# Kernel optimization log

Measured on AMD Instinct MI355X. Metric: run time of the kernel, lower is better.

Reference implementation:

```python
import jax, jax.numpy as jnp
import numpy as np

ALPHA = 0.5  # config_param['alpha']


def setup_inputs() -> dict:
    key = jax.random.key(0)
    ks = jax.random.split(key, 10)
    B, T, N, E, H = 64, 20, 8192, 128, 128
    # sparse multi-hot basket indicators
    x = (jax.random.uniform(ks[0], (B, T, N)) < 0.01).astype(jnp.float32)
    seq_len = jax.random.randint(ks[1], (B,), 1, T + 1)  # pack_padded requires >=1
    A = jax.random.uniform(ks[2], (N, N), dtype=jnp.float32) * 0.01  # dense item-item adjacency
    W1 = jax.random.normal(ks[3], (E, N), dtype=jnp.float32) * 0.02
    b1 = jnp.zeros((E,), jnp.float32)
    W2 = jax.random.normal(ks[4], (E, N), dtype=jnp.float32) * 0.02
    b2 = jnp.zeros((E,), jnp.float32)
    W_ih = jax.random.normal(ks[5], (4 * H, E), dtype=jnp.float32) * 0.05
    W_hh = jax.random.normal(ks[6], (4 * H, H), dtype=jnp.float32) * 0.05
    b_ih = jnp.zeros((4 * H,), jnp.float32)
    b_hh = jnp.zeros((4 * H,), jnp.float32)
    W_out = jax.random.normal(ks[7], (N, H), dtype=jnp.float32) * 0.02
    I_B = jnp.ones((N,), jnp.float32) / N  # item_probs-style bias init
    threshold = jnp.array([0.005], jnp.float32)  # adj_matrix.mean()
    return dict(x=x, seq_len=seq_len, A=A, W1=W1, b1=b1, W2=W2, b2=b2,
                W_ih=W_ih, W_hh=W_hh, b_ih=b_ih, b_hh=b_hh,
                W_out=W_out, I_B=I_B, threshold=threshold)


def reference(x, seq_len, A, W1, b1, W2, b2, W_ih, W_hh, b_ih, b_hh, W_out, I_B, threshold):
    B, T, N = x.shape
    H = W_hh.shape[1]
    xf = x.reshape(B * T, N)
    # two basket encoders, elementwise max combine (dropout = identity in eval)
    e1 = jax.nn.relu(xf @ W1.T + b1)
    e2 = jax.nn.relu(xf @ W2.T + b2)
    basket = jnp.maximum(e1, e2).reshape(B, T, -1)  # [B, T, E]

    # 1-layer LSTM (torch gate order i,f,g,o); packed variable-length seqs
    # emulated by freezing (h, c) once t >= seq_len, so h_n matches pack_padded.
    valid = jnp.arange(T)[:, None] < seq_len[None, :]  # [T, B]
    xs = basket.transpose(1, 0, 2)                     # [T, B, E]
    b = b_ih + b_hh

    def step(carry, inp):
        h, c = carry
        x_t, v = inp
        gates = x_t @ W_ih.T + h @ W_hh.T + b
        i, f, g, o = jnp.split(gates, 4, axis=-1)
        c_new = jax.nn.sigmoid(f) * c + jax.nn.sigmoid(i) * jnp.tanh(g)
        h_new = jax.nn.sigmoid(o) * jnp.tanh(c_new)
        m = v[:, None]
        return (jnp.where(m, h_new, h), jnp.where(m, c_new, c)), None

    h0 = jnp.zeros((B, H), x.dtype)
    c0 = jnp.zeros((B, H), x.dtype)
    (h_n, _), _ = jax.lax.scan(step, (h0, c0), (xs, valid))

    p = jax.nn.sigmoid(h_n @ W_out.T)  # [B, N]
    # mm(p, diag(relu(I_B))) is algebraically an elementwise scale
    predict = (1.0 - ALPHA) * p + ALPHA * (p * jax.nn.relu(I_B) + jax.nn.relu(p @ A))
    return predict
```

## Files before the change

kernel.cpp:

```cpp
#include <hip/hip_runtime.h>
#include <hip/hip_bf16.h>
#include <stdint.h>

#define B_ 64
#define T_ 20
#define N_ 8192
#define E_ 128
#define H_ 128
#define G4 512
#define SPLITK 8

typedef short bf16x8 __attribute__((ext_vector_type(8)));
typedef float f32x4 __attribute__((ext_vector_type(4)));

__device__ __forceinline__ float sigmoidf_(float x){ return 1.0f/(1.0f+expf(-x)); }

__device__ __forceinline__ unsigned short f2bf(float f){
  union { float f; uint32_t u; } v; v.f = f;
  uint32_t u = v.u;
  uint32_t r = (u + 0x7FFFu + ((u >> 16) & 1u)) >> 16;
  return (unsigned short)r;
}
__device__ __forceinline__ uint32_t pk2(float a, float b){
  return (uint32_t)f2bf(a) | ((uint32_t)f2bf(b) << 16);
}
__device__ __forceinline__ float bf2f(unsigned short s){
  union { uint32_t u; float f; } v; v.u = ((uint32_t)s) << 16; return v.f;
}

__global__ void k_transpose(const float* __restrict__ W1, const float* __restrict__ W2,
                            unsigned short* __restrict__ W12T){
  __shared__ float t1[128][33];
  __shared__ float t2[128][33];
  int n0 = blockIdx.x * 32;
  int tid = threadIdx.x;
  int nl = tid & 31, eg = tid >> 5;
  for (int i = 0; i < 16; i++){
    int e = eg * 16 + i;
    t1[e][nl] = W1[(size_t)e*N_ + n0 + nl];
    t2[e][nl] = W2[(size_t)e*N_ + n0 + nl];
  }
  __syncthreads();
  for (int n = 0; n < 32; n++){
    float v = (tid < 128) ? t1[tid][n] : t2[tid-128][n];
    W12T[(size_t)(n0+n)*256 + tid] = f2bf(v);
  }
}

__global__ void k_mlp(const float* __restrict__ x, const int* __restrict__ seq_len,
                      const unsigned short* __restrict__ W12T, const float* __restrict__ b1,
                      const float* __restrict__ b2, float* __restrict__ basket){
  int bt = blockIdx.x;
  int b = bt / T_, t = bt % T_;
  int tid = threadIdx.x;
  if (t >= seq_len[b]){
    if (tid < 128) basket[(size_t)bt*E_ + tid] = 0.f;
    return;
  }
  __shared__ int idxs[1024];
  __shared__ int cnt;
  __shared__ float e2s[128];
  if (tid == 0) cnt = 0;
  __syncthreads();
  const float4* xr = (const float4*)(x + (size_t)bt * N_);
  for (int i = 0; i < 8; i++){
    float4 v = xr[i*256 + tid];
    int base = (i*256 + tid)*4;
    if (v.x != 0.f){ int q = atomicAdd(&cnt,1); idxs[q] = base;   }
    if (v.y != 0.f){ int q = atomicAdd(&cnt,1); idxs[q] = base+1; }
    if (v.z != 0.f){ int q = atomicAdd(&cnt,1); idxs[q] = base+2; }
    if (v.w != 0.f){ int q = atomicAdd(&cnt,1); idxs[q] = base+3; }
  }
  __syncthreads();
  int m = cnt; if (m > 1024) m = 1024;
  float acc = (tid < 128) ? b1[tid] : b2[tid-128];
  int i = 0;
  for (; i + 8 <= m; i += 8){
    int j0 = idxs[i+0], j1 = idxs[i+1], j2 = idxs[i+2], j3 = idxs[i+3];
    int j4 = idxs[i+4], j5 = idxs[i+5], j6 = idxs[i+6], j7 = idxs[i+7];
    float v0 = bf2f(W12T[(size_t)j0*256 + tid]);
    float v1 = bf2f(W12T[(size_t)j1*256 + tid]);
    float v2 = bf2f(W12T[(size_t)j2*256 + tid]);
    float v3 = bf2f(W12T[(size_t)j3*256 + tid]);
    float v4 = bf2f(W12T[(size_t)j4*256 + tid]);
    float v5 = bf2f(W12T[(size_t)j5*256 + tid]);
    float v6 = bf2f(W12T[(size_t)j6*256 + tid]);
    float v7 = bf2f(W12T[(size_t)j7*256 + tid]);
    acc += ((v0+v1)+(v2+v3)) + ((v4+v5)+(v6+v7));
  }
  for (; i < m; i++)
    acc += bf2f(W12T[(size_t)idxs[i]*256 + tid]);
  acc = fmaxf(acc, 0.f);
  if (tid >= 128) e2s[tid-128] = acc;
  __syncthreads();
  if (tid < 128) basket[(size_t)bt*E_ + tid] = fmaxf(acc, e2s[tid]);
}

__global__ void k_xgemm(const float* __restrict__ basket, const float* __restrict__ W_ih,
                        const float* __restrict__ b_ih, const float* __restrict__ b_hh,
                        float* __restrict__ Xp){
  __shared__ unsigned short hb[64*128];
  int tid = threadIdx.x;
  int rt = blockIdx.x;
  int ct = blockIdx.y;
  {
    int row = tid >> 2;
    int k16 = (tid & 3) * 32;
    const float4* hr = (const float4*)(basket + ((size_t)rt*64 + row)*E_ + k16);
    #pragma unroll
    for (int i = 0; i < 4; i++){
      float4 a = hr[i*2], bq = hr[i*2+1];
      uint4 u; u.x = pk2(a.x,a.y); u.y = pk2(a.z,a.w); u.z = pk2(bq.x,bq.y); u.w = pk2(bq.z,bq.w);
      int blk = (k16 >> 3) + i;
      *(uint4*)&hb[row*128 + ((blk ^ (row & 7)) * 8)] = u;
    }
  }
  __syncthreads();
  int w = tid >> 6, l = tid & 63;
  int n0 = ct * 128;
  f32x4 acc[8];
  #pragma unroll
  for (int i = 0; i < 8; i++) acc[i] = (f32x4){0.f,0.f,0.f,0.f};
  int row = w*16 + (l & 15);
  #pragma unroll
  for (int ks = 0; ks < 4; ks++){
    int kk = ks*32 + (l >> 4)*8;
    int blk = kk >> 3;
    bf16x8 af = *(bf16x8*)&hb[row*128 + ((blk ^ (row & 7)) * 8)];
    #pragma unroll
    for (int nt = 0; nt < 8; nt++){
      int n = n0 + nt*16 + (l & 15);
      const float4* wp = (const float4*)(W_ih + (size_t)n*E_ + kk);
      float4 wa = wp[0], wb = wp[1];
      union { uint4 u; bf16x8 v; } cc;
      cc.u.x = pk2(wa.x,wa.y); cc.u.y = pk2(wa.z,wa.w);
      cc.u.z = pk2(wb.x,wb.y); cc.u.w = pk2(wb.z,wb.w);
      acc[nt] = __builtin_amdgcn_mfma_f32_16x16x32_bf16(af, cc.v, acc[nt], 0, 0, 0);
    }
  }
  #pragma unroll
  for (int nt = 0; nt < 8; nt++){
    int n = n0 + nt*16 + (l & 15);
    float bias = b_ih[n] + b_hh[n];
    #pragma unroll
    for (int r = 0; r < 4; r++){
      int rr = w*16 + (l >> 4)*4 + r;
      Xp[((size_t)rt*64 + rr)*G4 + n] = acc[nt][r] + bias;
    }
  }
}

__global__ void __launch_bounds__(512, 2)
k_lstm(const int* __restrict__ seq_len, const float* __restrict__ Xp,
       const float* __restrict__ W_hh, float* __restrict__ hn){
  int b = blockIdx.x;
  int L = seq_len[b];
  int j = threadIdx.x;
  float4 whh[32];
  const float4* wr = (const float4*)(W_hh + (size_t)j * H_);
  #pragma unroll
  for (int k = 0; k < 32; k++) whh[k] = wr[k];
  __shared__ float hs[128];
  __shared__ float gs[512];
  if (j < 128) hs[j] = 0.f;
  float c = 0.f;
  __syncthreads();
  for (int t = 0; t < L; t++){
    float s0 = Xp[((size_t)b*T_ + t)*G4 + j], s1 = 0.f, s2 = 0.f, s3 = 0.f;
    #pragma unroll
    for (int k = 0; k < 32; k += 4){
      float4 w, h;
      w = whh[k+0]; h = *(const float4*)&hs[k*4+ 0]; s0 += w.x*h.x + w.y*h.y + w.z*h.z + w.w*h.w;
      w = whh[k+1]; h = *(const float4*)&hs[k*4+ 4]; s1 += w.x*h.x + w.y*h.y + w.z*h.z + w.w*h.w;
      w = whh[k+2]; h = *(const float4*)&hs[k*4+ 8]; s2 += w.x*h.x + w.y*h.y + w.z*h.z + w.w*h.w;
      w = whh[k+3]; h = *(const float4*)&hs[k*4+12]; s3 += w.x*h.x + w.y*h.y + w.z*h.z + w.w*h.w;
    }
    gs[j] = (s0 + s1) + (s2 + s3);
    __syncthreads();
    if (j < 128){
      float i_ = gs[j], f_ = gs[128+j], gg = gs[256+j], o_ = gs[384+j];
      c = sigmoidf_(f_)*c + sigmoidf_(i_)*tanhf(gg);
      hs[j] = sigmoidf_(o_)*tanhf(c);
    }
    __syncthreads();
  }
  if (j < 128) hn[(size_t)b*H_ + j] = hs[j];
}

__global__ void k_pout(const float* __restrict__ hn, const float* __restrict__ W_out,
                       unsigned short* __restrict__ pbf){
  __shared__ unsigned short hb[64*128];
  int tid = threadIdx.x;
  {
    int row = tid >> 2;
    int k16 = (tid & 3) * 32;
    const float4* hr = (const float4*)(hn + (size_t)row*H_ + k16);
    #pragma unroll
    for (int i = 0; i < 4; i++){
      float4 a = hr[i*2], bq = hr[i*2+1];
      uint4 u; u.x = pk2(a.x,a.y); u.y = pk2(a.z,a.w); u.z = pk2(bq.x,bq.y); u.w = pk2(bq.z,bq.w);
      int blk = (k16 >> 3) + i;
      *(uint4*)&hb[row*128 + ((blk ^ (row & 7)) * 8)] = u;
    }
  }
  __syncthreads();
  int w = tid >> 6, l = tid & 63;
  int n0 = blockIdx.x * 128;
  f32x4 acc[8];
  #pragma unroll
  for (int i = 0; i < 8; i++) acc[i] = (f32x4){0.f,0.f,0.f,0.f};
  int row = w*16 + (l & 15);
  #pragma unroll
  for (int ks = 0; ks < 4; ks++){
    int kk = ks*32 + (l >> 4)*8;
    int blk = kk >> 3;
    bf16x8 af = *(bf16x8*)&hb[row*128 + ((blk ^ (row & 7)) * 8)];
    #pragma unroll
    for (int nt = 0; nt < 8; nt++){
      int n = n0 + nt*16 + (l & 15);
      const float4* wp = (const float4*)(W_out + (size_t)n*H_ + kk);
      float4 wa = wp[0], wb = wp[1];
      union { uint4 u; bf16x8 v; } cc;
      cc.u.x = pk2(wa.x,wa.y); cc.u.y = pk2(wa.z,wa.w);
      cc.u.z = pk2(wb.x,wb.y); cc.u.w = pk2(wb.z,wb.w);
      acc[nt] = __builtin_amdgcn_mfma_f32_16x16x32_bf16(af, cc.v, acc[nt], 0, 0, 0);
    }
  }
  #pragma unroll
  for (int nt = 0; nt < 8; nt++){
    int n = n0 + nt*16 + (l & 15);
    #pragma unroll
    for (int r = 0; r < 4; r++){
      int rr = w*16 + (l >> 4)*4 + r;
      float pv = 1.f/(1.f + expf(-acc[nt][r]));
      pbf[(size_t)rr*N_ + n] = f2bf(pv);
    }
  }
}

__global__ void __launch_bounds__(512, 4)
k_gemm(const unsigned short* __restrict__ pbf, const float* __restrict__ Ag,
       float* __restrict__ Cp){
  __shared__ unsigned short Abf0[128*64];
  __shared__ unsigned short Abf1[128*64];
  __shared__ unsigned short pt0[64*64];
  __shared__ unsigned short pt1[64*64];
  int tid = threadIdx.x;
  int nb = blockIdx.x & 63, ks = blockIdx.x >> 6;
  int n0 = nb * 128;
  int kbase = ks * (N_ / SPLITK);
  int sn = tid & 127, kq = tid >> 7;
  int prow = tid >> 3, c8 = tid & 7;
  int w = tid >> 6, l = tid & 63;
  int wm = w >> 2, wn = w & 3;
  f32x4 acc[2][2];
  #pragma unroll
  for (int i = 0; i < 2; i++)
    #pragma unroll
    for (int q = 0; q < 2; q++) acc[i][q] = (f32x4){0.f,0.f,0.f,0.f};
  float* Cout = Cp + (size_t)ks * (B_ * N_);
  const int NSTEP = (N_ / SPLITK) / 64;

  float aA[16], aB[16];
  uint4 pA, pB;

  auto issue = [&](float* ar, uint4& pr, int kb){
    pr = *(const uint4*)&pbf[(size_t)prow*N_ + kb + c8*8];
    #pragma unroll
    for (int i = 0; i < 4; i++){
      const float* base = Ag + (size_t)(kb + kq*16 + i*4)*N_ + n0 + sn;
      ar[i*4+0] = base[0];
      ar[i*4+1] = base[(size_t)N_];
      ar[i*4+2] = base[(size_t)2*N_];
      ar[i*4+3] = base[(size_t)3*N_];
    }
  };
  auto stage = [&](unsigned short* abf, unsigned short* ptb, const float* ar, const uint4& pr){
    *(uint4*)&ptb[prow*64 + ((c8*8) ^ ((prow & 7)*8))] = pr;
    #pragma unroll
    for (int i = 0; i < 4; i++){
      int k = kq*16 + i*4;
      uint2 u; u.x = pk2(ar[i*4+0], ar[i*4+1]); u.y = pk2(ar[i*4+2], ar[i*4+3]);
      *(uint2*)&abf[sn*64 + (k ^ ((sn & 7)*8))] = u;
    }
  };
  auto compute = [&](const unsigned short* abf, const unsigned short* ptb){
    #pragma unroll
    for (int kc = 0; kc < 64; kc += 32){
      int ko = kc + (l >> 4)*8;
      bf16x8 af[2], bfr[2];
      #pragma unroll
      for (int mi = 0; mi < 2; mi++){
        int r = wm*32 + mi*16 + (l & 15);
        af[mi] = *(const bf16x8*)&ptb[r*64 + (ko ^ ((r & 7)*8))];
      }
      #pragma unroll
      for (int ni = 0; ni < 2; ni++){
        int n = wn*32 + ni*16 + (l & 15);
        bfr[ni] = *(const bf16x8*)&abf[n*64 + (ko ^ ((n & 7)*8))];
      }
      #pragma unroll
      for (int mi = 0; mi < 2; mi++)
        #pragma unroll
        for (int ni = 0; ni < 2; ni++)
          acc[mi][ni] = __builtin_amdgcn_mfma_f32_16x16x32_bf16(af[mi], bfr[ni], acc[mi][ni], 0, 0, 0);
    }
  };

  issue(aA, pA, kbase);
  for (int s = 0; s < NSTEP; s += 2){
    if (s + 1 < NSTEP) issue(aB, pB, kbase + (s+1)*64);
    stage(Abf0, pt0, aA, pA);
    asm volatile("s_waitcnt lgkmcnt(0)" ::: "memory");
    __builtin_amdgcn_sched_barrier(0);
    __builtin_amdgcn_s_barrier();
    __builtin_amdgcn_sched_barrier(0);
    compute(Abf0, pt0);
    if (s + 2 < NSTEP) issue(aA, pA, kbase + (s+2)*64);
    stage(Abf1, pt1, aB, pB);
    asm volatile("s_waitcnt lgkmcnt(0)" ::: "memory");
    __builtin_amdgcn_sched_barrier(0);
    __builtin_amdgcn_s_barrier();
    __builtin_amdgcn_sched_barrier(0);
    compute(Abf1, pt1);
  }

  #pragma unroll
  for (int mi = 0; mi < 2; mi++)
    #pragma unroll
    for (int ni = 0; ni < 2; ni++){
      int n = n0 + wn*32 + ni*16 + (l & 15);
      #pragma unroll
      for (int r = 0; r < 4; r++){
        int rr = wm*32 + mi*16 + (l >> 4)*4 + r;
        Cout[(size_t)rr*N_ + n] = acc[mi][ni][r];
      }
    }
}

__global__ void k_final(const unsigned short* __restrict__ pbf, const float* __restrict__ Cp,
                        const float* __restrict__ I_B, float* __restrict__ out){
  int idx = blockIdx.x*256 + threadIdx.x;
  ushort4 pu = ((const ushort4*)pbf)[idx];
  float4 cv = {0.f, 0.f, 0.f, 0.f};
  #pragma unroll
  for (int s = 0; s < SPLITK; s++){
    float4 v = ((const float4*)(Cp + (size_t)s * (B_ * N_)))[idx];
    cv.x += v.x; cv.y += v.y; cv.z += v.z; cv.w += v.w;
  }
  int n = (idx*4) & (N_-1);
  float4 ib = *(const float4*)&I_B[n];
  float4 o;
  float p0 = bf2f(pu.x), p1 = bf2f(pu.y), p2 = bf2f(pu.z), p3 = bf2f(pu.w);
  o.x = 0.5f*p0 + 0.5f*(p0*fmaxf(ib.x,0.f) + fmaxf(cv.x,0.f));
  o.y = 0.5f*p1 + 0.5f*(p1*fmaxf(ib.y,0.f) + fmaxf(cv.y,0.f));
  o.z = 0.5f*p2 + 0.5f*(p2*fmaxf(ib.z,0.f) + fmaxf(cv.z,0.f));
  o.w = 0.5f*p3 + 0.5f*(p3*fmaxf(ib.w,0.f) + fmaxf(cv.w,0.f));
  ((float4*)out)[idx] = o;
}

extern "C" void kernel_launch(void* const* d_in, const int* in_sizes, int n_in,
                              void* d_out, int out_size, void* d_ws, size_t ws_size,
                              hipStream_t stream) {
  const float* x     = (const float*)d_in[0];
  const int*   seq   = (const int*)  d_in[1];
  const float* A     = (const float*)d_in[2];
  const float* W1    = (const float*)d_in[3];
  const float* b1    = (const float*)d_in[4];
  const float* W2    = (const float*)d_in[5];
  const float* b2    = (const float*)d_in[6];
  const float* W_ih  = (const float*)d_in[7];
  const float* W_hh  = (const float*)d_in[8];
  const float* b_ih  = (const float*)d_in[9];
  const float* b_hh  = (const float*)d_in[10];
  const float* W_out = (const float*)d_in[11];
  const float* I_B   = (const float*)d_in[12];
  float* out = (float*)d_out;

  float* ws   = (float*)d_ws;
  unsigned short* W12T = (unsigned short*)ws;
  float* basket = ws + 1048576;
  float* Xp     = basket + 163840;
  float* hn     = Xp + 655360;
  float* Cp     = hn + 8192;
  unsigned short* pbf = (unsigned short*)(Cp + 4194304);

  k_transpose<<<256, 256, 0, stream>>>(W1, W2, W12T);
  k_mlp      <<<1280,256, 0, stream>>>(x, seq, W12T, b1, b2, basket);
  k_xgemm    <<<dim3(20,4), 256, 0, stream>>>(basket, W_ih, b_ih, b_hh, Xp);
  k_lstm     <<<64,  512, 0, stream>>>(seq, Xp, W_hh, hn);
  k_pout     <<<64,  256, 0, stream>>>(hn, W_out, pbf);
  k_gemm     <<<64*SPLITK, 512, 0, stream>>>(pbf, A, Cp);
  k_final    <<<512, 256, 0, stream>>>(pbf, Cp, I_B, out);
}
```

Before: 152.5 us.

## Fuse input projection into LSTM kernel and split-K reduction into GEMM

The separate MFMA input-projection GEMM is removed. Each LSTM block now computes its own 20x512 input gates in fp32 from shared-memory basket rows and keeps them in LDS. The final epilogue kernel is folded into the main GEMM through a per-column-tile atomic semaphore, so the last split-K block reduces the partial sums and writes the output. This saves two kernel launches and the Xp round trip through global memory, in exchange for more serial scalar work per LSTM block, heavy register pressure, and a tail reduction done by a few blocks.

```diff
diff --git a/kernel.cpp b/kernel.cpp
--- a/kernel.cpp
+++ b/kernel.cpp
@@ -29,7 +29,8 @@
 }
 
 __global__ void k_transpose(const float* __restrict__ W1, const float* __restrict__ W2,
-                            unsigned short* __restrict__ W12T){
+                            unsigned short* __restrict__ W12T, unsigned* __restrict__ sems){
+  if (blockIdx.x == 0 && threadIdx.x < 64) sems[threadIdx.x] = 0;
   __shared__ float t1[128][33];
   __shared__ float t2[128][33];
   int n0 = blockIdx.x * 32;
@@ -96,77 +97,47 @@
   if (tid < 128) basket[(size_t)bt*E_ + tid] = fmaxf(acc, e2s[tid]);
 }
 
-__global__ void k_xgemm(const float* __restrict__ basket, const float* __restrict__ W_ih,
-                        const float* __restrict__ b_ih, const float* __restrict__ b_hh,
-                        float* __restrict__ Xp){
-  __shared__ unsigned short hb[64*128];
-  int tid = threadIdx.x;
-  int rt = blockIdx.x;
-  int ct = blockIdx.y;
-  {
-    int row = tid >> 2;
-    int k16 = (tid & 3) * 32;
-    const float4* hr = (const float4*)(basket + ((size_t)rt*64 + row)*E_ + k16);
-    #pragma unroll
-    for (int i = 0; i < 4; i++){
-      float4 a = hr[i*2], bq = hr[i*2+1];
-      uint4 u; u.x = pk2(a.x,a.y); u.y = pk2(a.z,a.w); u.z = pk2(bq.x,bq.y); u.w = pk2(bq.z,bq.w);
-      int blk = (k16 >> 3) + i;
-      *(uint4*)&hb[row*128 + ((blk ^ (row & 7)) * 8)] = u;
-    }
-  }
-  __syncthreads();
-  int w = tid >> 6, l = tid & 63;
-  int n0 = ct * 128;
-  f32x4 acc[8];
-  #pragma unroll
-  for (int i = 0; i < 8; i++) acc[i] = (f32x4){0.f,0.f,0.f,0.f};
-  int row = w*16 + (l & 15);
-  #pragma unroll
-  for (int ks = 0; ks < 4; ks++){
-    int kk = ks*32 + (l >> 4)*8;
-    int blk = kk >> 3;
-    bf16x8 af = *(bf16x8*)&hb[row*128 + ((blk ^ (row & 7)) * 8)];
-    #pragma unroll
-    for (int nt = 0; nt < 8; nt++){
-      int n = n0 + nt*16 + (l & 15);
-      const float4* wp = (const float4*)(W_ih + (size_t)n*E_ + kk);
-      float4 wa = wp[0], wb = wp[1];
-      union { uint4 u; bf16x8 v; } cc;
-      cc.u.x = pk2(wa.x,wa.y); cc.u.y = pk2(wa.z,wa.w);
-      cc.u.z = pk2(wb.x,wb.y); cc.u.w = pk2(wb.z,wb.w);
-      acc[nt] = __builtin_amdgcn_mfma_f32_16x16x32_bf16(af, cc.v, acc[nt], 0, 0, 0);
-    }
-  }
-  #pragma unroll
-  for (int nt = 0; nt < 8; nt++){
-    int n = n0 + nt*16 + (l & 15);
-    float bias = b_ih[n] + b_hh[n];
-    #pragma unroll
-    for (int r = 0; r < 4; r++){
-      int rr = w*16 + (l >> 4)*4 + r;
-      Xp[((size_t)rt*64 + rr)*G4 + n] = acc[nt][r] + bias;
-    }
-  }
-}
-
-__global__ void __launch_bounds__(512, 2)
-k_lstm(const int* __restrict__ seq_len, const float* __restrict__ Xp,
-       const float* __restrict__ W_hh, float* __restrict__ hn){
+__global__ void __launch_bounds__(512, 1)
+k_lstmx(const int* __restrict__ seq_len, const float* __restrict__ basket,
+        const float* __restrict__ W_ih, const float* __restrict__ b_ih,
+        const float* __restrict__ b_hh, const float* __restrict__ W_hh,
+        float* __restrict__ hn){
   int b = blockIdx.x;
   int L = seq_len[b];
   int j = threadIdx.x;
-  float4 whh[32];
-  const float4* wr = (const float4*)(W_hh + (size_t)j * H_);
-  #pragma unroll
-  for (int k = 0; k < 32; k++) whh[k] = wr[k];
+  __shared__ float bsk[T_][E_];
+  __shared__ float XpL[T_][G4];
   __shared__ float hs[128];
   __shared__ float gs[512];
+  for (int idx = j; idx < T_*E_; idx += 512)
+    bsk[idx>>7][idx&127] = basket[((size_t)b*T_ + (idx>>7))*E_ + (idx&127)];
+  __syncthreads();
+  {
+    float bias = b_ih[j] + b_hh[j];
+    float accv[T_];
+    #pragma unroll
+    for (int tt = 0; tt < T_; tt++) accv[tt] = bias;
+    const float4* wr = (const float4*)(W_ih + (size_t)j * E_);
+    for (int k4 = 0; k4 < 32; k4++){
+      float4 w = wr[k4];
+      #pragma unroll
+      for (int tt = 0; tt < T_; tt++){
+        float4 h = *(const float4*)&bsk[tt][k4*4];
+        accv[tt] += w.x*h.x + w.y*h.y + w.z*h.z + w.w*h.w;
+      }
+    }
+    #pragma unroll
+    for (int tt = 0; tt < T_; tt++) XpL[tt][j] = accv[tt];
+  }
+  float4 whh[32];
+  const float4* wr2 = (const float4*)(W_hh + (size_t)j * H_);
+  #pragma unroll
+  for (int k = 0; k < 32; k++) whh[k] = wr2[k];
   if (j < 128) hs[j] = 0.f;
   float c = 0.f;
   __syncthreads();
   for (int t = 0; t < L; t++){
-    float s0 = Xp[((size_t)b*T_ + t)*G4 + j], s1 = 0.f, s2 = 0.f, s3 = 0.f;
+    float s0 = XpL[t][j], s1 = 0.f, s2 = 0.f, s3 = 0.f;
     #pragma unroll
     for (int k = 0; k < 32; k += 4){
       float4 w, h;
@@ -239,12 +210,14 @@
 }
 
 __global__ void __launch_bounds__(512, 4)
-k_gemm(const unsigned short* __restrict__ pbf, const float* __restrict__ Ag,
-       float* __restrict__ Cp){
+k_gemmf(const unsigned short* __restrict__ pbf, const float* __restrict__ Ag,
+        float* __restrict__ Cp, const float* __restrict__ I_B,
+        float* __restrict__ out, unsigned* __restrict__ sems){
   __shared__ unsigned short Abf0[128*64];
   __shared__ unsigned short Abf1[128*64];
   __shared__ unsigned short pt0[64*64];
   __shared__ unsigned short pt1[64*64];
+  __shared__ unsigned lastf;
   int tid = threadIdx.x;
   int nb = blockIdx.x & 63, ks = blockIdx.x >> 6;
   int n0 = nb * 128;
@@ -336,27 +309,38 @@
         Cout[(size_t)rr*N_ + n] = acc[mi][ni][r];
       }
     }
-}
-
-__global__ void k_final(const unsigned short* __restrict__ pbf, const float* __restrict__ Cp,
-                        const float* __restrict__ I_B, float* __restrict__ out){
-  int idx = blockIdx.x*256 + threadIdx.x;
-  ushort4 pu = ((const ushort4*)pbf)[idx];
-  float4 cv = {0.f, 0.f, 0.f, 0.f};
-  #pragma unroll
-  for (int s = 0; s < SPLITK; s++){
-    float4 v = ((const float4*)(Cp + (size_t)s * (B_ * N_)))[idx];
-    cv.x += v.x; cv.y += v.y; cv.z += v.z; cv.w += v.w;
-  }
-  int n = (idx*4) & (N_-1);
-  float4 ib = *(const float4*)&I_B[n];
-  float4 o;
-  float p0 = bf2f(pu.x), p1 = bf2f(pu.y), p2 = bf2f(pu.z), p3 = bf2f(pu.w);
-  o.x = 0.5f*p0 + 0.5f*(p0*fmaxf(ib.x,0.f) + fmaxf(cv.x,0.f));
-  o.y = 0.5f*p1 + 0.5f*(p1*fmaxf(ib.y,0.f) + fmaxf(cv.y,0.f));
-  o.z = 0.5f*p2 + 0.5f*(p2*fmaxf(ib.z,0.f) + fmaxf(cv.z,0.f));
-  o.w = 0.5f*p3 + 0.5f*(p3*fmaxf(ib.w,0.f) + fmaxf(cv.w,0.f));
-  ((float4*)out)[idx] = o;
+
+  __threadfence();
+  __syncthreads();
+  if (tid == 0){
+    unsigned old = atomicAdd(&sems[nb], 1);
+    lastf = (old == SPLITK-1) ? 1u : 0u;
+  }
+  __syncthreads();
+  if (lastf){
+    __threadfence();
+    #pragma unroll
+    for (int g = 0; g < 4; g++){
+      int e = g*512 + tid;
+      int row = e >> 5, c4 = e & 31;
+      size_t off = (size_t)row*N_ + n0 + c4*4;
+      float4 cv = {0.f,0.f,0.f,0.f};
+      #pragma unroll
+      for (int s2 = 0; s2 < SPLITK; s2++){
+        float4 v = *(const float4*)&Cp[(size_t)s2*(B_*N_) + off];
+        cv.x += v.x; cv.y += v.y; cv.z += v.z; cv.w += v.w;
+      }
+      ushort4 pu = *(const ushort4*)&pbf[off];
+      float4 ib = *(const float4*)&I_B[n0 + c4*4];
+      float p0 = bf2f(pu.x), p1 = bf2f(pu.y), p2 = bf2f(pu.z), p3 = bf2f(pu.w);
+      float4 o;
+      o.x = 0.5f*p0 + 0.5f*(p0*fmaxf(ib.x,0.f) + fmaxf(cv.x,0.f));
+      o.y = 0.5f*p1 + 0.5f*(p1*fmaxf(ib.y,0.f) + fmaxf(cv.y,0.f));
+      o.z = 0.5f*p2 + 0.5f*(p2*fmaxf(ib.z,0.f) + fmaxf(cv.z,0.f));
+      o.w = 0.5f*p3 + 0.5f*(p3*fmaxf(ib.w,0.f) + fmaxf(cv.w,0.f));
+      *(float4*)&out[off] = o;
+    }
+  }
 }
 
 extern "C" void kernel_launch(void* const* d_in, const int* in_sizes, int n_in,
@@ -377,19 +361,17 @@
   const float* I_B   = (const float*)d_in[12];
   float* out = (float*)d_out;
 
-  float* ws   = (float*)d_ws;
+  float* ws = (float*)d_ws;
   unsigned short* W12T = (unsigned short*)ws;
   float* basket = ws + 1048576;
-  float* Xp     = basket + 163840;
-  float* hn     = Xp + 655360;
+  float* hn     = basket + 163840;
   float* Cp     = hn + 8192;
   unsigned short* pbf = (unsigned short*)(Cp + 4194304);
-
-  k_transpose<<<256, 256, 0, stream>>>(W1, W2, W12T);
+  unsigned* sems = (unsigned*)(Cp + 4194304 + 262144);
+
+  k_transpose<<<256, 256, 0, stream>>>(W1, W2, W12T, sems);
   k_mlp      <<<1280,256, 0, stream>>>(x, seq, W12T, b1, b2, basket);
-  k_xgemm    <<<dim3(20,4), 256, 0, stream>>>(basket, W_ih, b_ih, b_hh, Xp);
-  k_lstm     <<<64,  512, 0, stream>>>(seq, Xp, W_hh, hn);
+  k_lstmx    <<<64,  512, 0, stream>>>(seq, basket, W_ih, b_ih, b_hh, W_hh, hn);
   k_pout     <<<64,  256, 0, stream>>>(hn, W_out, pbf);
-  k_gemm     <<<64*SPLITK, 512, 0, stream>>>(pbf, A, Cp);
-  k_final    <<<512, 256, 0, stream>>>(pbf, Cp, I_B, out);
-}
+  k_gemmf    <<<64*SPLITK, 512, 0, stream>>>(pbf, A, Cp, I_B, out, sems);
+}
```

Measured after the change: 294.3 us. 93.0% more time.
